# Performance work log

Hardware: AMD Instinct MI355X
Metric: run time of the kernel (lower is better)

Reference implementation:

```python
import jax, jax.numpy as jnp
import numpy as np

HALF = 6          # half window size from the source (y±6, x±6)
MAX_COORD = 63    # clamp max from the source
N_KPT = 21
MOMENTUM = 0.999  # m in forward; val2 initialized to 0.0 after reset()


def _box_means(f, pre):
    """Per-keypoint box mean, then mean over batch. f: [B,C,H,W], pre: [B,21,2] int.
    Matches torch slicing feature[:, left:right, down:upper] (exclusive upper bounds)."""
    b, c, h, w = f.shape
    fm = f.mean(axis=1)                                   # [B,H,W] (mean over C commutes with spatial mean)
    x = pre[..., 0]
    y = pre[..., 1]
    left = jnp.clip(x - HALF, 0, None).astype(jnp.int32)   # [B,21]
    right = jnp.clip(x + HALF, None, MAX_COORD).astype(jnp.int32)
    down = jnp.clip(y - HALF, 0, None).astype(jnp.int32)
    upper = jnp.clip(y + HALF, None, MAX_COORD).astype(jnp.int32)
    rows = jnp.arange(h)
    cols = jnp.arange(w)
    rmask = ((rows >= left[..., None]) & (rows < right[..., None])).astype(f.dtype)   # [B,21,H]
    cmask = ((cols >= down[..., None]) & (cols < upper[..., None])).astype(f.dtype)   # [B,21,W]
    cnt = ((right - left) * (upper - down)).astype(f.dtype)                           # [B,21]
    sums = jnp.einsum('bhw,bkh,bkw->bk', fm, rmask, cmask)                            # [B,21]
    return (sums / cnt).mean(axis=0)                                                  # [21]


def setup_inputs() -> dict:
    key = jax.random.key(0)
    k1, k2, k3, k4 = jax.random.split(key, 4)
    B, C, H, W = 64, 256, 64, 64
    return {
        'f1': jax.random.normal(k1, (B, C, H, W), dtype=jnp.float32),
        'f2': jax.random.normal(k2, (B, C, H, W), dtype=jnp.float32),
        'pre1': jax.random.randint(k3, (B, N_KPT, 2), 0, 64, dtype=jnp.int32),
        'pre2': jax.random.randint(k4, (B, N_KPT, 2), 0, 64, dtype=jnp.int32),
    }


def reference(f1, f2, pre1, pre2):
    fea_c1 = _box_means(f1, pre1)                  # [21]
    fea_c2 = MOMENTUM * _box_means(f2, pre2)       # val2 == 0.0 initially, so (1-m)*val2 == 0
    return jnp.mean((fea_c1 - fea_c2) ** 2)        # MSELoss(reduction='mean')
```

## Files before the change

kernel.cpp:

```cpp
#include <hip/hip_runtime.h>

#define B   64
#define C   256
#define H   64
#define W   64
#define HW  (H * W)
#define KPT 21

__global__ __launch_bounds__(256) void channel_mean_kernel(
    const float* __restrict__ f1, const float* __restrict__ f2,
    float* __restrict__ fm)
{
    const float* f  = blockIdx.y ? f2 : f1;
    float* out      = fm + (size_t)blockIdx.y * B * HW;

    const int b     = blockIdx.x >> 2;
    const int pix0  = ((blockIdx.x & 3) * 256 + threadIdx.x) * 4;
    const float* base = f + (size_t)b * C * HW + pix0;

    float4 acc = make_float4(0.f, 0.f, 0.f, 0.f);
    #pragma unroll 8
    for (int c = 0; c < C; ++c) {
        const float4 v = *(const float4*)(base + (size_t)c * HW);
        acc.x += v.x; acc.y += v.y; acc.z += v.z; acc.w += v.w;
    }
    const float inv = 1.0f / (float)C;
    float4 o = make_float4(acc.x * inv, acc.y * inv, acc.z * inv, acc.w * inv);
    *(float4*)(out + (size_t)b * HW + pix0) = o;
}

__global__ __launch_bounds__(128) void box_mean_kernel(
    const float* __restrict__ fm,
    const int* __restrict__ pre1, const int* __restrict__ pre2,
    float* __restrict__ feas)
{
    const int k    = blockIdx.x;
    const int lane = threadIdx.x & 63;
    const int wave = threadIdx.x >> 6;
    const int b    = lane;

    const int* pre = wave ? pre2 : pre1;
    const float* base = fm + (size_t)wave * B * HW + (size_t)b * HW;

    const int x = pre[(b * KPT + k) * 2 + 0];
    const int y = pre[(b * KPT + k) * 2 + 1];
    const int l = max(x - 6, 0);
    const int r = min(x + 6, 63);
    const int d = max(y - 6, 0);
    const int u = min(y + 6, 63);

    float s = 0.f;
    for (int row = l; row < r; ++row) {
        const float* rp = base + row * W;
        for (int col = d; col < u; ++col)
            s += rp[col];
    }
    float mean = s / (float)((r - l) * (u - d));

    #pragma unroll
    for (int off = 32; off > 0; off >>= 1)
        mean += __shfl_down(mean, off, 64);

    if (lane == 0)
        feas[wave * KPT + k] = mean * (1.0f / (float)B);
}

__global__ __launch_bounds__(64) void final_mse_kernel(
    const float* __restrict__ feas, float* __restrict__ out)
{
    const int k = threadIdx.x;
    float v = 0.f;
    if (k < KPT) {
        const float diff = feas[k] - 0.999f * feas[KPT + k];
        v = diff * diff;
    }
    #pragma unroll
    for (int off = 32; off > 0; off >>= 1)
        v += __shfl_down(v, off, 64);
    if (threadIdx.x == 0)
        out[0] = v * (1.0f / (float)KPT);
}

extern "C" void kernel_launch(void* const* d_in, const int* in_sizes, int n_in,
                              void* d_out, int out_size, void* d_ws, size_t ws_size,
                              hipStream_t stream)
{
    const float* f1  = (const float*)d_in[0];
    const float* f2  = (const float*)d_in[1];
    const int*  pre1 = (const int*)d_in[2];
    const int*  pre2 = (const int*)d_in[3];

    float* fm   = (float*)d_ws;
    float* feas = fm + 2 * B * HW;

    channel_mean_kernel<<<dim3(B * 4, 2), 256, 0, stream>>>(f1, f2, fm);
    box_mean_kernel<<<KPT, 128, 0, stream>>>(fm, pre1, pre2, feas);
    final_mse_kernel<<<1, 64, 0, stream>>>(feas, (float*)d_out);
}
```

Measured before the change: 535.7 us.

## Skip channel reduction for pixels outside keypoint boxes; parallelize box sums

The channel-mean kernel first checks whether each thread's 4-pixel group overlaps any of the 21 keypoint boxes for its batch. It only streams the 256 channels (with nontemporal loads) when the group is needed, which cuts HBM traffic for uncovered pixels. The box-mean kernel now uses 4 lanes per batch with vector loads over a fixed 12-row window and a block reduction, replacing a serial per-thread loop. Each thread gains 21 keypoint checks and its memory access pattern becomes divergent.

```diff
diff --git a/kernel.cpp b/kernel.cpp
--- a/kernel.cpp
+++ b/kernel.cpp
@@ -7,40 +7,62 @@
 #define HW  (H * W)
 #define KPT 21
 
+typedef float f32x4 __attribute__((ext_vector_type(4)));
+
 __global__ __launch_bounds__(256) void channel_mean_kernel(
     const float* __restrict__ f1, const float* __restrict__ f2,
+    const int* __restrict__ pre1, const int* __restrict__ pre2,
     float* __restrict__ fm)
 {
-    const float* f  = blockIdx.y ? f2 : f1;
-    float* out      = fm + (size_t)blockIdx.y * B * HW;
+    const int t = blockIdx.y;
+    const float* __restrict__ f  = t ? f2 : f1;
+    const int* __restrict__ pre  = t ? pre2 : pre1;
+    float* out = fm + (size_t)t * B * HW;
 
-    const int b     = blockIdx.x >> 2;
-    const int pix0  = ((blockIdx.x & 3) * 256 + threadIdx.x) * 4;
-    const float* base = f + (size_t)b * C * HW + pix0;
+    const int b    = blockIdx.x >> 2;
+    const int pix0 = ((blockIdx.x & 3) * 256 + threadIdx.x) * 4;
+    const int row  = pix0 >> 6;
+    const int col0 = pix0 & 63;
 
-    float4 acc = make_float4(0.f, 0.f, 0.f, 0.f);
-    #pragma unroll 8
-    for (int c = 0; c < C; ++c) {
-        const float4 v = *(const float4*)(base + (size_t)c * HW);
-        acc.x += v.x; acc.y += v.y; acc.z += v.z; acc.w += v.w;
+    bool needed = false;
+    #pragma unroll
+    for (int k = 0; k < KPT; ++k) {
+        const int x = pre[(b * KPT + k) * 2 + 0];
+        const int y = pre[(b * KPT + k) * 2 + 1];
+        const int l = max(x - 6, 0);
+        const int r = min(x + 6, 63);
+        const int d = max(y - 6, 0);
+        const int u = min(y + 6, 63);
+        const bool hit = (row >= l) && (row < r) && (col0 < u) && (col0 + 4 > d);
+        needed = needed || hit;
     }
-    const float inv = 1.0f / (float)C;
-    float4 o = make_float4(acc.x * inv, acc.y * inv, acc.z * inv, acc.w * inv);
-    *(float4*)(out + (size_t)b * HW + pix0) = o;
+
+    f32x4 acc = {0.f, 0.f, 0.f, 0.f};
+    if (needed) {
+        const float* base = f + (size_t)b * (C * HW) + pix0;
+        #pragma unroll 16
+        for (int c = 0; c < C; ++c) {
+            const f32x4 v =
+                __builtin_nontemporal_load((const f32x4*)(base + (size_t)c * HW));
+            acc += v;
+        }
+    }
+    acc *= (1.0f / (float)C);
+    *(f32x4*)(out + (size_t)b * HW + pix0) = acc;
 }
 
-__global__ __launch_bounds__(128) void box_mean_kernel(
+__global__ __launch_bounds__(256) void box_mean_kernel(
     const float* __restrict__ fm,
     const int* __restrict__ pre1, const int* __restrict__ pre2,
     float* __restrict__ feas)
 {
-    const int k    = blockIdx.x;
-    const int lane = threadIdx.x & 63;
-    const int wave = threadIdx.x >> 6;
-    const int b    = lane;
+    const int k = blockIdx.x;
+    const int t = blockIdx.y;
+    const int j = threadIdx.x & 3;
+    const int b = threadIdx.x >> 2;
 
-    const int* pre = wave ? pre2 : pre1;
-    const float* base = fm + (size_t)wave * B * HW + (size_t)b * HW;
+    const int* __restrict__ pre = t ? pre2 : pre1;
+    const float* base = fm + ((size_t)t * B + b) * HW;
 
     const int x = pre[(b * KPT + k) * 2 + 0];
     const int y = pre[(b * KPT + k) * 2 + 1];
@@ -49,20 +71,40 @@
     const int d = max(y - 6, 0);
     const int u = min(y + 6, 63);
 
+    const int g0  = (d >> 2) + j;
+    const bool okg = g0 < 16;
+    const int g   = okg ? g0 : 15;
+    const int c0  = g * 4;
+
     float s = 0.f;
-    for (int row = l; row < r; ++row) {
-        const float* rp = base + row * W;
-        for (int col = d; col < u; ++col)
-            s += rp[col];
+    #pragma unroll
+    for (int i = 0; i < 12; ++i) {
+        const int rw  = l + i;
+        const int rwc = rw < 63 ? rw : 63;
+        const f32x4 v = *(const f32x4*)(base + rwc * W + c0);
+        const bool okr = okg && (rw < r);
+        #pragma unroll
+        for (int cc = 0; cc < 4; ++cc) {
+            const int col = c0 + cc;
+            s += (okr && (col >= d) && (col < u)) ? v[cc] : 0.f;
+        }
     }
-    float mean = s / (float)((r - l) * (u - d));
 
+    s += __shfl_xor(s, 1, 64);
+    s += __shfl_xor(s, 2, 64);
+    const float mean = s / (float)((r - l) * (u - d));
+
+    float vsum = mean;
     #pragma unroll
-    for (int off = 32; off > 0; off >>= 1)
-        mean += __shfl_down(mean, off, 64);
+    for (int off = 4; off < 64; off <<= 1)
+        vsum += __shfl_xor(vsum, off, 64);
 
-    if (lane == 0)
-        feas[wave * KPT + k] = mean * (1.0f / (float)B);
+    __shared__ float part[4];
+    const int wave = threadIdx.x >> 6;
+    if ((threadIdx.x & 63) == 0) part[wave] = vsum;
+    __syncthreads();
+    if (threadIdx.x == 0)
+        feas[t * KPT + k] = (part[0] + part[1] + part[2] + part[3]) * (1.0f / (float)B);
 }
 
 __global__ __launch_bounds__(64) void final_mse_kernel(
@@ -93,7 +135,7 @@
     float* fm   = (float*)d_ws;
     float* feas = fm + 2 * B * HW;
 
-    channel_mean_kernel<<<dim3(B * 4, 2), 256, 0, stream>>>(f1, f2, fm);
-    box_mean_kernel<<<KPT, 128, 0, stream>>>(fm, pre1, pre2, feas);
+    channel_mean_kernel<<<dim3(B * 4, 2), 256, 0, stream>>>(f1, f2, pre1, pre2, fm);
+    box_mean_kernel<<<dim3(KPT, 2), 256, 0, stream>>>(fm, pre1, pre2, feas);
     final_mse_kernel<<<1, 64, 0, stream>>>(feas, (float*)d_out);
 }
```

After: 476.1 us (median of 2 runs). -11.1%, faster.
